# Kernel tuning notes

Measured on AMD Instinct MI355X. Metric: run time of the kernel, lower is better.

The kernel has to match this reference:

```python
import jax, jax.numpy as jnp
import numpy as np

W0, W1 = 8, 8           # attn_grid_window_size
HEADS = 8
ATTN_CH = 256
HD = ATTN_CH // HEADS   # 32
LN_EPS = 1e-5
L2_EPS = 1e-12


def _rel_pos_index(h, w):
    # Swin-style relative position index, [h*w, h*w] int
    coords = np.stack(np.meshgrid(np.arange(h), np.arange(w), indexing='ij'))  # [2,h,w]
    coords = coords.reshape(2, -1)                                             # [2,L]
    rel = coords[:, :, None] - coords[:, None, :]                              # [2,L,L]
    rel = rel.transpose(1, 2, 0).astype(np.int64)                              # [L,L,2]
    rel[:, :, 0] += h - 1
    rel[:, :, 1] += w - 1
    rel[:, :, 0] *= 2 * w - 1
    return rel.sum(-1)                                                         # [L,L]

_REL_IDX = _rel_pos_index(W0, W1)


def _layernorm2d(x, g, b):
    # nn.LayerNorm((8,8)): normalize over the last two dims, affine shape (8,8)
    mu = jnp.mean(x, axis=(-2, -1), keepdims=True)
    var = jnp.var(x, axis=(-2, -1), keepdims=True)
    return (x - mu) * jax.lax.rsqrt(var + LN_EPS) * g + b


def setup_inputs() -> dict:
    key = jax.random.key(0)
    ks = jax.random.split(key, 8)
    C = 256
    return {
        'X': jax.random.normal(ks[0], (8, C, 128, 128), jnp.float32),
        'pre_gamma': jnp.ones((W0, W1), jnp.float32),
        'pre_beta': jnp.zeros((W0, W1), jnp.float32),
        'post_gamma': jnp.ones((W0, W1), jnp.float32),
        'post_beta': jnp.zeros((W0, W1), jnp.float32),
        'Wqkv': jax.random.normal(ks[1], (3 * ATTN_CH, C), jnp.float32) * 0.02,
        'bqkv': jnp.zeros((3 * ATTN_CH,), jnp.float32),
        'Wproj': jax.random.normal(ks[2], (C, ATTN_CH), jnp.float32) * 0.02,
        'bproj': jnp.zeros((C,), jnp.float32),
        'rel_bias_table': jax.random.normal(ks[3], ((2 * W0 - 1) * (2 * W1 - 1), HEADS), jnp.float32) * 0.02,
    }


def reference(X, pre_gamma, pre_beta, post_gamma, post_beta,
              Wqkv, bqkv, Wproj, bproj, rel_bias_table):
    N, C, H, W = X.shape
    L = W0 * W1
    # --- block partition (mirrors torch view/permute/contiguous().view) ---
    xp = X.reshape(N, C, H // W0, W0, W // W1, W1)
    xp = xp.transpose(0, 2, 4, 3, 5, 1).reshape(-1, C, W0, W1)  # [Bw, C, 8, 8]
    Bw = xp.shape[0]
    # --- pre-norm over the window dims ---
    xn = _layernorm2d(xp, pre_gamma, pre_beta)
    # --- windowed multi-head self-attention with relative position bias ---
    x = xn.reshape(Bw, C, L)
    qkv = jnp.einsum('oc,bcl->bol', Wqkv, x) + bqkv[None, :, None]   # [Bw, 3A, L]
    qkv = qkv.reshape(Bw, 3, HEADS, HD, L)
    q = qkv[:, 0].transpose(0, 1, 3, 2)  # [Bw, h, L, d]
    k = qkv[:, 1].transpose(0, 1, 3, 2)
    v = qkv[:, 2].transpose(0, 1, 3, 2)
    # MetNet-3 qk normalization (L2 normalize instead of 1/sqrt(d) scale)
    q = q / jnp.clip(jnp.linalg.norm(q, axis=-1, keepdims=True), L2_EPS)
    k = k / jnp.clip(jnp.linalg.norm(k, axis=-1, keepdims=True), L2_EPS)
    bias = rel_bias_table[jnp.asarray(_REL_IDX)].transpose(2, 0, 1)  # [h, L, L]
    attn = jnp.einsum('bhld,bhmd->bhlm', q, k) + bias[None]          # [Bw, h, L, L]
    attn = jax.nn.softmax(attn, axis=-1)
    out = jnp.einsum('bhlm,bhmd->bhld', attn, v)                     # [Bw, h, L, d]
    out = out.transpose(0, 1, 3, 2).reshape(Bw, ATTN_CH, L)          # [Bw, A, L]
    out = jnp.einsum('ca,bal->bcl', Wproj, out) + bproj[None, :, None]
    out = out.reshape(Bw, C, W0, W1)
    # --- residual, post-norm + Identity MLP residual ---
    y = xp + out
    y = y + _layernorm2d(y, post_gamma, post_beta)
    # --- reverse partition: composition of torch .view()s == plain reshape ---
    return y.reshape(N, C, H, W)
```

## Files before the change

kernel.cpp:

```cpp
#include <hip/hip_runtime.h>

typedef __bf16 bf16x8 __attribute__((ext_vector_type(8)));
typedef float  f32x4  __attribute__((ext_vector_type(4)));

#define DEVI static __device__ __forceinline__

#define LDS_FENCE() do { \
  asm volatile("s_waitcnt lgkmcnt(0)" ::: "memory"); \
  __builtin_amdgcn_sched_barrier(0); \
} while (0)

DEVI unsigned short f2bf(float f) {
  __bf16 h = (__bf16)f;
  return __builtin_bit_cast(unsigned short, h);
}
DEVI float bf2f(unsigned short s) {
  union { unsigned u; float f; } v; v.u = ((unsigned)s) << 16;
  return v.f;
}

__global__ void prep_kernel(const float* __restrict__ Wqkv, const float* __restrict__ Wproj,
                            const float* __restrict__ table,
                            unsigned short* __restrict__ wq, unsigned short* __restrict__ wp,
                            float* __restrict__ biasg, float* __restrict__ rowsum) {
  const int i = blockIdx.x * 256 + threadIdx.x;
  if (i < 768 * 256) wq[i] = f2bf(Wqkv[i]);
  if (i < 256 * 256) wp[i] = f2bf(Wproj[i]);
  if (i < 8 * 64 * 64) {
    const int h = i >> 12, r = (i >> 6) & 63, c = i & 63;
    const int ridx = ((r >> 3) - (c >> 3) + 7) * 15 + ((r & 7) - (c & 7) + 7);
    biasg[i] = table[ridx * 8 + h];
  }
  if (i < 768) {
    const float4* p = reinterpret_cast<const float4*>(Wqkv + (size_t)i * 256);
    float s = 0.f;
#pragma unroll
    for (int j = 0; j < 64; ++j) { const float4 a = p[j]; s += a.x + a.y + a.z + a.w; }
    rowsum[i] = s;
  }
}

#define LDS_XN  0u
#define LDS_ST  32768u
#define LDS_XW  34816u
#define LDS_SCR 34816u
#define LDS_TOTAL 104448u

__global__ void __launch_bounds__(512, 2)
win_attn_kernel(const float* __restrict__ X,
                const float* __restrict__ preg, const float* __restrict__ preb,
                const float* __restrict__ postg, const float* __restrict__ postb,
                const float* __restrict__ bqkv, const float* __restrict__ bproj,
                const unsigned short* __restrict__ wq, const unsigned short* __restrict__ wp,
                const float* __restrict__ biasg, const float* __restrict__ rowsum,
                float* __restrict__ out) {
  __shared__ alignas(16) unsigned char sh[LDS_TOTAL];
  const int tid = threadIdx.x;
  const int w = tid >> 6;
  const int lane = tid & 63, lm = lane & 15, lg = lane >> 4;
  const int orig = blockIdx.x;
  const int b = (orig & 7) * 256 + (orig >> 3);
  const int n = b >> 8, gh = (b >> 4) & 15, gw = b & 15;
  const size_t wbase = (size_t)n * 4194304 + (size_t)gh * 1024 + (size_t)gw * 8;

  {
#pragma unroll
    for (int i = 0; i < 4; ++i) {
      const int rid = i * 512 + tid;
      const int cc = rid >> 3, w0 = rid & 7;
      const float* xb = X + wbase + (size_t)cc * 16384 + w0 * 128;
      const float4 a  = *reinterpret_cast<const float4*>(xb);
      const float4 bv = *reinterpret_cast<const float4*>(xb + 4);
      const unsigned xorv = (cc & 64) ? 16u : 0u;
      unsigned char* dst = sh + LDS_XW + (unsigned)cc * 272u + (unsigned)w0 * 32u;
      *reinterpret_cast<float4*>(dst + xorv)         = a;
      *reinterpret_cast<float4*>(dst + (16u ^ xorv)) = bv;
    }
  }
  __syncthreads();

  {
    const int c = tid >> 1, half = tid & 1;
    const int r = ((c >> 5) << 3) + ((c >> 2) & 7);
    const unsigned base = LDS_XW + (unsigned)(c & 3) * (64u * 272u)
                        + 4u * (unsigned)(r ^ ((c & 1) << 2));
    float fv[32];
    float s1 = 0.f, s2 = 0.f;
#pragma unroll
    for (int i = 0; i < 32; ++i) {
      const int l = half * 32 + i;
      const float v = *reinterpret_cast<const float*>(sh + base + (unsigned)l * 272u);
      fv[i] = v; s1 += v; s2 += v * v;
    }
    s1 += __shfl_xor(s1, 1);
    s2 += __shfl_xor(s2, 1);
    const float mean = s1 * (1.f / 64.f);
    float var = s2 * (1.f / 64.f) - mean * mean;
    var = fmaxf(var, 0.f) + 1e-5f;
    const float rstd = rsqrtf(var);
    const float sig  = var * rstd;
#pragma unroll
    for (int i = 0; i < 32; ++i) {
      const int l = half * 32 + i;
      *(unsigned short*)(sh + LDS_XN + l * 512 +
          (((unsigned)(2 * c)) ^ ((unsigned)((l & 7) << 4)))) = f2bf((fv[i] - mean) * rstd);
    }
    if (!half) *reinterpret_cast<float2*>(sh + LDS_ST + c * 8) = float2{mean, sig};
  }
  const unsigned char* wqb = (const unsigned char*)wq;
  size_t aoff[6];
  bf16x8 acur[6];
#pragma unroll
  for (int t = 0; t < 6; ++t) {
    const int o = (t >> 1) * 256 + 32 * w + 16 * (t & 1) + lm;
    aoff[t] = (size_t)o * 512 + lg * 16;
    acur[t] = *reinterpret_cast<const bf16x8*>(wqb + aoff[t]);
  }
  __syncthreads();

  float pg4[4], pb4[4];
#pragma unroll
  for (int nt = 0; nt < 4; ++nt) { pg4[nt] = preg[nt * 16 + lm]; pb4[nt] = preb[nt * 16 + lm]; }
  f32x4 acc6[6][4];
#pragma unroll
  for (int t = 0; t < 6; ++t)
#pragma unroll
    for (int j = 0; j < 4; ++j) acc6[t][j] = f32x4{0.f, 0.f, 0.f, 0.f};
#pragma unroll
  for (int ks = 0; ks < 8; ++ks) {
    bf16x8 anxt[6];
    if (ks < 7) {
#pragma unroll
      for (int t = 0; t < 6; ++t)
        anxt[t] = *reinterpret_cast<const bf16x8*>(wqb + aoff[t] + (ks + 1) * 64);
    }
    bf16x8 bfrag[4];
#pragma unroll
    for (int nt = 0; nt < 4; ++nt) {
      const int l = nt * 16 + lm;
      bfrag[nt] = *reinterpret_cast<const bf16x8*>(
          sh + LDS_XN + l * 512 + (((unsigned)(ks * 64 + lg * 16)) ^ ((unsigned)((l & 7) << 4))));
    }
#pragma unroll
    for (int t = 0; t < 6; ++t)
#pragma unroll
      for (int nt = 0; nt < 4; ++nt)
        acc6[t][nt] = __builtin_amdgcn_mfma_f32_16x16x32_bf16(acur[t], bfrag[nt], acc6[t][nt], 0, 0, 0);
    if (ks < 7) {
#pragma unroll
      for (int t = 0; t < 6; ++t) acur[t] = anxt[t];
    }
  }
#pragma unroll
  for (int t = 0; t < 6; ++t) {
    const int ob = (t >> 1) * 256 + 32 * w + 16 * (t & 1);
    const f32x4 rs4 = *reinterpret_cast<const f32x4*>(rowsum + ob + lg * 4);
    const f32x4 bq4 = *reinterpret_cast<const f32x4*>(bqkv   + ob + lg * 4);
#pragma unroll
    for (int nt = 0; nt < 4; ++nt)
#pragma unroll
      for (int reg = 0; reg < 4; ++reg)
        acc6[t][nt][reg] = pg4[nt] * acc6[t][nt][reg] + pb4[nt] * rs4[reg] + bq4[reg];
  }
#pragma unroll
  for (int sec = 0; sec < 2; ++sec)
#pragma unroll
    for (int nt = 0; nt < 4; ++nt) {
      float ss = 0.f;
#pragma unroll
      for (int sub = 0; sub < 2; ++sub)
#pragma unroll
        for (int reg = 0; reg < 4; ++reg) {
          const float v = acc6[2 * sec + sub][nt][reg];
          ss += v * v;
        }
      ss += __shfl_xor(ss, 16);
      ss += __shfl_xor(ss, 32);
      const float inv = 1.f / fmaxf(sqrtf(ss), 1e-12f);
#pragma unroll
      for (int sub = 0; sub < 2; ++sub)
#pragma unroll
        for (int reg = 0; reg < 4; ++reg)
          acc6[2 * sec + sub][nt][reg] *= inv;
    }

  const unsigned scr = LDS_SCR + (unsigned)w * 4608u;
  bf16x8 qfrag[4], kfrag[4];
#pragma unroll
  for (int nt = 0; nt < 4; ++nt) {
    bf16x8 qv, kv;
#pragma unroll
    for (int sub = 0; sub < 2; ++sub)
#pragma unroll
      for (int reg = 0; reg < 4; ++reg) {
        qv[sub * 4 + reg] = (__bf16)acc6[sub][nt][reg];
        kv[sub * 4 + reg] = (__bf16)acc6[2 + sub][nt][reg];
      }
    qfrag[nt] = qv; kfrag[nt] = kv;
  }
#pragma unroll
  for (int sub = 0; sub < 2; ++sub)
#pragma unroll
    for (int reg = 0; reg < 4; ++reg) {
      const int d = 16 * sub + 4 * lg + reg;
#pragma unroll
      for (int nt = 0; nt < 4; ++nt) {
        const int pcol = (nt >> 1) * 32 + (lm >> 2) * 8 + (nt & 1) * 4 + (lm & 3);
        *(unsigned short*)(sh + scr + (unsigned)(d * 144 + 2 * pcol)) =
            f2bf(acc6[4 + sub][nt][reg]);
      }
    }
  LDS_FENCE();
  bf16x8 vf[2][2];
#pragma unroll
  for (int ks = 0; ks < 2; ++ks)
#pragma unroll
    for (int mtd = 0; mtd < 2; ++mtd)
      vf[ks][mtd] = *reinterpret_cast<const bf16x8*>(
          sh + scr + (unsigned)((mtd * 16 + lm) * 144 + ks * 64 + lg * 16));
  LDS_FENCE();

  const float* bh = biasg + w * 4096;
  f32x4 oaccT[2][4];
#pragma unroll
  for (int mtd = 0; mtd < 2; ++mtd)
#pragma unroll
    for (int nt = 0; nt < 4; ++nt) oaccT[mtd][nt] = f32x4{0.f, 0.f, 0.f, 0.f};
#pragma unroll
  for (int nt = 0; nt < 4; ++nt) {
    f32x4 bb[4];
#pragma unroll
    for (int mt = 0; mt < 4; ++mt)
      bb[mt] = *reinterpret_cast<const f32x4*>(bh + (nt * 16 + lm) * 64 + mt * 16 + 4 * lg);
    f32x4 st[4];
#pragma unroll
    for (int mt = 0; mt < 4; ++mt)
      st[mt] = __builtin_amdgcn_mfma_f32_16x16x32_bf16(kfrag[mt], qfrag[nt],
                                                       f32x4{0.f,0.f,0.f,0.f}, 0, 0, 0);
    float mmax = -1e30f;
#pragma unroll
    for (int mt = 0; mt < 4; ++mt)
#pragma unroll
      for (int reg = 0; reg < 4; ++reg) {
        st[mt][reg] += bb[mt][reg];
        mmax = fmaxf(mmax, st[mt][reg]);
      }
    mmax = fmaxf(mmax, __shfl_xor(mmax, 16));
    mmax = fmaxf(mmax, __shfl_xor(mmax, 32));
    float sum = 0.f;
#pragma unroll
    for (int mt = 0; mt < 4; ++mt)
#pragma unroll
      for (int reg = 0; reg < 4; ++reg) {
        const float e = __expf(st[mt][reg] - mmax);
        st[mt][reg] = e;
        sum += e;
      }
    sum += __shfl_xor(sum, 16);
    sum += __shfl_xor(sum, 32);
    const float rinv = 1.f / sum;
#pragma unroll
    for (int ks = 0; ks < 2; ++ks) {
      bf16x8 pf;
#pragma unroll
      for (int sub = 0; sub < 2; ++sub)
#pragma unroll
        for (int reg = 0; reg < 4; ++reg)
          pf[sub * 4 + reg] = (__bf16)(st[2 * ks + sub][reg] * rinv);
#pragma unroll
      for (int mtd = 0; mtd < 2; ++mtd)
        oaccT[mtd][nt] = __builtin_amdgcn_mfma_f32_16x16x32_bf16(vf[ks][mtd], pf,
                                                                 oaccT[mtd][nt], 0, 0, 0);
    }
  }
#pragma unroll
  for (int mtd = 0; mtd < 2; ++mtd)
#pragma unroll
    for (int reg = 0; reg < 4; ++reg) {
      const int d = mtd * 16 + 4 * lg + reg;
#pragma unroll
      for (int nt = 0; nt < 4; ++nt)
        *(unsigned short*)(sh + scr + (unsigned)((nt * 16 + lm) * 64 + 2 * d)) =
            f2bf(oaccT[mtd][nt][reg]);
    }

  const unsigned char* wpb = (const unsigned char*)wp;
  size_t poff[2];
  bf16x8 pcur[2];
#pragma unroll
  for (int mt = 0; mt < 2; ++mt) {
    poff[mt] = (size_t)(w * 32 + mt * 16 + lm) * 512 + lg * 16;
    pcur[mt] = *reinterpret_cast<const bf16x8*>(wpb + poff[mt]);
  }
  __syncthreads();

  {
    float pog4[4], pob4[4];
#pragma unroll
    for (int nt = 0; nt < 4; ++nt) { pog4[nt] = postg[nt * 16 + lm]; pob4[nt] = postb[nt * 16 + lm]; }
    f32x4 pacc[2][4];
#pragma unroll
    for (int i = 0; i < 2; ++i)
#pragma unroll
      for (int j = 0; j < 4; ++j) pacc[i][j] = f32x4{0.f, 0.f, 0.f, 0.f};
#pragma unroll
    for (int ks = 0; ks < 8; ++ks) {
      bf16x8 pnxt[2];
      if (ks < 7) {
#pragma unroll
        for (int mt = 0; mt < 2; ++mt)
          pnxt[mt] = *reinterpret_cast<const bf16x8*>(wpb + poff[mt] + (ks + 1) * 64);
      }
      bf16x8 bfr[4];
#pragma unroll
      for (int nt = 0; nt < 4; ++nt)
        bfr[nt] = *reinterpret_cast<const bf16x8*>(
            sh + LDS_SCR + (unsigned)(ks * 4608 + (nt * 16 + lm) * 64 + lg * 16));
#pragma unroll
      for (int mt = 0; mt < 2; ++mt)
#pragma unroll
        for (int nt = 0; nt < 4; ++nt)
          pacc[mt][nt] = __builtin_amdgcn_mfma_f32_16x16x32_bf16(pcur[mt], bfr[nt], pacc[mt][nt], 0, 0, 0);
      if (ks < 7) {
#pragma unroll
        for (int mt = 0; mt < 2; ++mt) pcur[mt] = pnxt[mt];
      }
    }
#pragma unroll
    for (int mt = 0; mt < 2; ++mt) {
      const float4 bp4 = *reinterpret_cast<const float4*>(bproj + w * 32 + mt * 16 + lg * 4);
#pragma unroll
      for (int reg = 0; reg < 4; ++reg) {
        const int c = w * 32 + mt * 16 + lg * 4 + reg;
        const float bp = ((const float*)&bp4)[reg];
        const float2 ms = *reinterpret_cast<const float2*>(sh + LDS_ST + c * 8);
        float y[4];
        float s1 = 0.f, s2 = 0.f;
#pragma unroll
        for (int nt = 0; nt < 4; ++nt) {
          const int l = nt * 16 + lm;
          const float xh = bf2f(*(const unsigned short*)(
              sh + LDS_XN + l * 512 + (((unsigned)(2 * c)) ^ ((unsigned)((l & 7) << 4)))));
          const float v = xh * ms.y + ms.x + pacc[mt][nt][reg] + bp;
          y[nt] = v;
          s1 += v; s2 += v * v;
        }
        s1 += __shfl_xor(s1, 1); s2 += __shfl_xor(s2, 1);
        s1 += __shfl_xor(s1, 2); s2 += __shfl_xor(s2, 2);
        s1 += __shfl_xor(s1, 4); s2 += __shfl_xor(s2, 4);
        s1 += __shfl_xor(s1, 8); s2 += __shfl_xor(s2, 8);
        const float mean = s1 * (1.f / 64.f);
        const float var  = s2 * (1.f / 64.f) - mean * mean;
        const float rstd = rsqrtf(fmaxf(var, 0.f) + 1e-5f);
        float* orow = out + (size_t)b * 16384 + (size_t)c * 64;
#pragma unroll
        for (int nt = 0; nt < 4; ++nt) {
          const float v = y[nt];
          orow[nt * 16 + lm] = v + (v - mean) * rstd * pog4[nt] + pob4[nt];
        }
      }
    }
  }
}

extern "C" void kernel_launch(void* const* d_in, const int* in_sizes, int n_in,
                              void* d_out, int out_size, void* d_ws, size_t ws_size,
                              hipStream_t stream) {
  const float* X     = (const float*)d_in[0];
  const float* preg  = (const float*)d_in[1];
  const float* preb  = (const float*)d_in[2];
  const float* postg = (const float*)d_in[3];
  const float* postb = (const float*)d_in[4];
  const float* Wqkv  = (const float*)d_in[5];
  const float* bqkv  = (const float*)d_in[6];
  const float* Wproj = (const float*)d_in[7];
  const float* bproj = (const float*)d_in[8];
  const float* table = (const float*)d_in[9];

  unsigned short* wq = (unsigned short*)d_ws;
  unsigned short* wp = (unsigned short*)((char*)d_ws + 393216);
  float* biasg       = (float*)((char*)d_ws + 524288);
  float* rowsum      = (float*)((char*)d_ws + 655360);

  prep_kernel<<<768, 256, 0, stream>>>(Wqkv, Wproj, table, wq, wp, biasg, rowsum);
  win_attn_kernel<<<2048, 512, 0, stream>>>(X, preg, preb, postg, postb,
                                            bqkv, bproj, wq, wp, biasg, rowsum,
                                            (float*)d_out);
}
```

Before: 259.2 us.

## Keep input window in registers and compute LayerNorm stats via shuffles

The staging of the raw fp32 window tile in LDS is removed. Each thread now holds its 32 input values in registers, and the pre-LayerNorm partial sums are reduced with cross-lane shuffles plus a small LDS partial-sum table before the normalized bf16 tile is written. This cuts the kernel's LDS footprint from about 104 KB to 72 KB, which should let two 512-thread blocks share a CU as the launch bounds request. The cost is two extra block barriers, more register pressure from holding the tile, and a wider per-channel stats record in LDS.

```diff
diff --git a/kernel.cpp b/kernel.cpp
--- a/kernel.cpp
+++ b/kernel.cpp
@@ -42,9 +42,8 @@
 
 #define LDS_XN  0u
 #define LDS_ST  32768u
-#define LDS_XW  34816u
-#define LDS_SCR 34816u
-#define LDS_TOTAL 104448u
+#define LDS_SCR 36864u
+#define LDS_TOTAL 73728u
 
 __global__ void __launch_bounds__(512, 2)
 win_attn_kernel(const float* __restrict__ X,
@@ -63,50 +62,58 @@
   const int n = b >> 8, gh = (b >> 4) & 15, gw = b & 15;
   const size_t wbase = (size_t)n * 4194304 + (size_t)gh * 1024 + (size_t)gw * 8;
 
-  {
-#pragma unroll
-    for (int i = 0; i < 4; ++i) {
-      const int rid = i * 512 + tid;
-      const int cc = rid >> 3, w0 = rid & 7;
-      const float* xb = X + wbase + (size_t)cc * 16384 + w0 * 128;
-      const float4 a  = *reinterpret_cast<const float4*>(xb);
-      const float4 bv = *reinterpret_cast<const float4*>(xb + 4);
-      const unsigned xorv = (cc & 64) ? 16u : 0u;
-      unsigned char* dst = sh + LDS_XW + (unsigned)cc * 272u + (unsigned)w0 * 32u;
-      *reinterpret_cast<float4*>(dst + xorv)         = a;
-      *reinterpret_cast<float4*>(dst + (16u ^ xorv)) = bv;
-    }
-  }
+  const int l0 = tid >> 3, w0 = tid & 7;
+  float fv[4][8];
+#pragma unroll
+  for (int i = 0; i < 4; ++i) {
+    const int cc = i * 64 + l0;
+    const float* xb = X + wbase + (size_t)cc * 16384 + w0 * 128;
+    const float4 a  = *reinterpret_cast<const float4*>(xb);
+    const float4 bv = *reinterpret_cast<const float4*>(xb + 4);
+    fv[i][0] = a.x;  fv[i][1] = a.y;  fv[i][2] = a.z;  fv[i][3] = a.w;
+    fv[i][4] = bv.x; fv[i][5] = bv.y; fv[i][6] = bv.z; fv[i][7] = bv.w;
+  }
+#pragma unroll
+  for (int i = 0; i < 4; ++i)
+#pragma unroll
+    for (int j = 0; j < 8; ++j) {
+      float s = fv[i][j];
+      float q = s * s;
+      s += __shfl_xor(s, 8);  q += __shfl_xor(q, 8);
+      s += __shfl_xor(s, 16); q += __shfl_xor(q, 16);
+      s += __shfl_xor(s, 32); q += __shfl_xor(q, 32);
+      if (lane < 8) {
+        const int c = lane * 32 + j * 4 + i;
+        *reinterpret_cast<float2*>(sh + LDS_SCR + (unsigned)(c * 64 + w * 8)) = float2{s, q};
+      }
+    }
   __syncthreads();
 
-  {
-    const int c = tid >> 1, half = tid & 1;
-    const int r = ((c >> 5) << 3) + ((c >> 2) & 7);
-    const unsigned base = LDS_XW + (unsigned)(c & 3) * (64u * 272u)
-                        + 4u * (unsigned)(r ^ ((c & 1) << 2));
-    float fv[32];
-    float s1 = 0.f, s2 = 0.f;
-#pragma unroll
-    for (int i = 0; i < 32; ++i) {
-      const int l = half * 32 + i;
-      const float v = *reinterpret_cast<const float*>(sh + base + (unsigned)l * 272u);
-      fv[i] = v; s1 += v; s2 += v * v;
-    }
-    s1 += __shfl_xor(s1, 1);
-    s2 += __shfl_xor(s2, 1);
+  if (tid < 256) {
+    const int c = tid;
+    const float4 p0 = *reinterpret_cast<const float4*>(sh + LDS_SCR + (unsigned)(c * 64));
+    const float4 p1 = *reinterpret_cast<const float4*>(sh + LDS_SCR + (unsigned)(c * 64 + 16));
+    const float4 p2 = *reinterpret_cast<const float4*>(sh + LDS_SCR + (unsigned)(c * 64 + 32));
+    const float4 p3 = *reinterpret_cast<const float4*>(sh + LDS_SCR + (unsigned)(c * 64 + 48));
+    const float s1 = p0.x + p0.z + p1.x + p1.z + p2.x + p2.z + p3.x + p3.z;
+    const float s2 = p0.y + p0.w + p1.y + p1.w + p2.y + p2.w + p3.y + p3.w;
     const float mean = s1 * (1.f / 64.f);
-    float var = s2 * (1.f / 64.f) - mean * mean;
-    var = fmaxf(var, 0.f) + 1e-5f;
+    float var = fmaxf(s2 * (1.f / 64.f) - mean * mean, 0.f) + 1e-5f;
     const float rstd = rsqrtf(var);
     const float sig  = var * rstd;
-#pragma unroll
-    for (int i = 0; i < 32; ++i) {
-      const int l = half * 32 + i;
-      *(unsigned short*)(sh + LDS_XN + l * 512 +
-          (((unsigned)(2 * c)) ^ ((unsigned)((l & 7) << 4)))) = f2bf((fv[i] - mean) * rstd);
-    }
-    if (!half) *reinterpret_cast<float2*>(sh + LDS_ST + c * 8) = float2{mean, sig};
-  }
+    *reinterpret_cast<float4*>(sh + LDS_ST + (unsigned)(c * 16)) = float4{mean, sig, rstd, 0.f};
+  }
+  __syncthreads();
+
+#pragma unroll
+  for (int i = 0; i < 4; ++i)
+#pragma unroll
+    for (int j = 0; j < 8; ++j) {
+      const int c = w0 * 32 + j * 4 + i;
+      const float4 st = *reinterpret_cast<const float4*>(sh + LDS_ST + (unsigned)(c * 16));
+      *(unsigned short*)(sh + LDS_XN + l0 * 512 +
+          (((unsigned)(2 * c)) ^ ((unsigned)((l0 & 7) << 4)))) = f2bf((fv[i][j] - st.x) * st.z);
+    }
   const unsigned char* wqb = (const unsigned char*)wq;
   size_t aoff[6];
   bf16x8 acur[6];
@@ -333,7 +340,7 @@
       for (int reg = 0; reg < 4; ++reg) {
         const int c = w * 32 + mt * 16 + lg * 4 + reg;
         const float bp = ((const float*)&bp4)[reg];
-        const float2 ms = *reinterpret_cast<const float2*>(sh + LDS_ST + c * 8);
+        const float4 ms4 = *reinterpret_cast<const float4*>(sh + LDS_ST + (unsigned)(c * 16));
         float y[4];
         float s1 = 0.f, s2 = 0.f;
 #pragma unroll
@@ -341,7 +348,7 @@
           const int l = nt * 16 + lm;
           const float xh = bf2f(*(const unsigned short*)(
               sh + LDS_XN + l * 512 + (((unsigned)(2 * c)) ^ ((unsigned)((l & 7) << 4)))));
-          const float v = xh * ms.y + ms.x + pacc[mt][nt][reg] + bp;
+          const float v = xh * ms4.y + ms4.x + pacc[mt][nt][reg] + bp;
           y[nt] = v;
           s1 += v; s2 += v * v;
         }
```

Result: slower. 310.8 us (+19.9%).

## Load window input directly from global, dropping LDS staging buffer

Applied to the files above, without the earlier changes.

Removes the coalesced float4 staging of the input window into a padded LDS transpose buffer. Each thread now reads its 32 strided channel values for the pre-LayerNorm straight from global memory. This shrinks the shared-memory footprint from about 104 KB to about 74 KB, which should let two 512-thread blocks fit per CU, and it drops one barrier. In exchange the global loads are scalar and strided, touching only 32-byte contiguous segments per group of lanes. The per-channel stats slot is also widened to a float4 that stores rstd.

```diff
diff --git a/kernel.cpp b/kernel.cpp
--- a/kernel.cpp
+++ b/kernel.cpp
@@ -42,9 +42,8 @@
 
 #define LDS_XN  0u
 #define LDS_ST  32768u
-#define LDS_XW  34816u
-#define LDS_SCR 34816u
-#define LDS_TOTAL 104448u
+#define LDS_SCR 36864u
+#define LDS_TOTAL 73728u
 
 __global__ void __launch_bounds__(512, 2)
 win_attn_kernel(const float* __restrict__ X,
@@ -64,48 +63,32 @@
   const size_t wbase = (size_t)n * 4194304 + (size_t)gh * 1024 + (size_t)gw * 8;
 
   {
-#pragma unroll
-    for (int i = 0; i < 4; ++i) {
-      const int rid = i * 512 + tid;
-      const int cc = rid >> 3, w0 = rid & 7;
-      const float* xb = X + wbase + (size_t)cc * 16384 + w0 * 128;
-      const float4 a  = *reinterpret_cast<const float4*>(xb);
-      const float4 bv = *reinterpret_cast<const float4*>(xb + 4);
-      const unsigned xorv = (cc & 64) ? 16u : 0u;
-      unsigned char* dst = sh + LDS_XW + (unsigned)cc * 272u + (unsigned)w0 * 32u;
-      *reinterpret_cast<float4*>(dst + xorv)         = a;
-      *reinterpret_cast<float4*>(dst + (16u ^ xorv)) = bv;
-    }
-  }
-  __syncthreads();
-
-  {
     const int c = tid >> 1, half = tid & 1;
-    const int r = ((c >> 5) << 3) + ((c >> 2) & 7);
-    const unsigned base = LDS_XW + (unsigned)(c & 3) * (64u * 272u)
-                        + 4u * (unsigned)(r ^ ((c & 1) << 2));
+    const float* xb = X + wbase
+                    + ((size_t)((c & 3) * 64 + half * 32)) * 16384
+                    + (c >> 5) * 128 + ((c >> 2) & 7);
     float fv[32];
     float s1 = 0.f, s2 = 0.f;
 #pragma unroll
     for (int i = 0; i < 32; ++i) {
-      const int l = half * 32 + i;
-      const float v = *reinterpret_cast<const float*>(sh + base + (unsigned)l * 272u);
+      const float v = xb[(size_t)i * 16384];
       fv[i] = v; s1 += v; s2 += v * v;
     }
     s1 += __shfl_xor(s1, 1);
     s2 += __shfl_xor(s2, 1);
     const float mean = s1 * (1.f / 64.f);
-    float var = s2 * (1.f / 64.f) - mean * mean;
-    var = fmaxf(var, 0.f) + 1e-5f;
+    float var = fmaxf(s2 * (1.f / 64.f) - mean * mean, 0.f) + 1e-5f;
     const float rstd = rsqrtf(var);
     const float sig  = var * rstd;
+    const unsigned colb = (unsigned)(2 * c);
 #pragma unroll
     for (int i = 0; i < 32; ++i) {
       const int l = half * 32 + i;
       *(unsigned short*)(sh + LDS_XN + l * 512 +
-          (((unsigned)(2 * c)) ^ ((unsigned)((l & 7) << 4)))) = f2bf((fv[i] - mean) * rstd);
-    }
-    if (!half) *reinterpret_cast<float2*>(sh + LDS_ST + c * 8) = float2{mean, sig};
+          (colb ^ ((unsigned)((l & 7) << 4)))) = f2bf((fv[i] - mean) * rstd);
+    }
+    if (!half)
+      *reinterpret_cast<float4*>(sh + LDS_ST + (unsigned)(c * 16)) = float4{mean, sig, rstd, 0.f};
   }
   const unsigned char* wqb = (const unsigned char*)wq;
   size_t aoff[6];
@@ -333,7 +316,7 @@
       for (int reg = 0; reg < 4; ++reg) {
         const int c = w * 32 + mt * 16 + lg * 4 + reg;
         const float bp = ((const float*)&bp4)[reg];
-        const float2 ms = *reinterpret_cast<const float2*>(sh + LDS_ST + c * 8);
+        const float4 ms4 = *reinterpret_cast<const float4*>(sh + LDS_ST + (unsigned)(c * 16));
         float y[4];
         float s1 = 0.f, s2 = 0.f;
 #pragma unroll
@@ -341,7 +324,7 @@
           const int l = nt * 16 + lm;
           const float xh = bf2f(*(const unsigned short*)(
               sh + LDS_XN + l * 512 + (((unsigned)(2 * c)) ^ ((unsigned)((l & 7) << 4)))));
-          const float v = xh * ms.y + ms.x + pacc[mt][nt][reg] + bp;
+          const float v = xh * ms4.y + ms4.x + pacc[mt][nt][reg] + bp;
           y[nt] = v;
           s1 += v; s2 += v * v;
         }
```

New measurement: 267.5 us. 3.2% more time.
